# Kernel tuning notes

Measured on AMD Instinct MI355X. Metric: run time of the kernel, lower is better.

## Reference

```python
import jax, jax.numpy as jnp
import numpy as np

GAMMA = 2          # relu(cos_sim)**gamma, from init gamma=2
EPS = 1e-8         # torch CosineSimilarity eps (norm clamp)
B, C, H, WID = 4, 256, 64, 64


def setup_inputs() -> dict:
    key = jax.random.key(0)
    kx, kw = jax.random.split(key)
    x = jax.random.normal(kx, (B, C, H, WID), dtype=jnp.float32)
    # 1x1 conv (nlayers=1): weight [C_out, C_in], bias [C_out]
    W = jax.random.normal(kw, (C, C), dtype=jnp.float32) * 0.02
    b = jnp.zeros((C,), dtype=jnp.float32)
    return {"x": x, "W": W, "b": b}


def reference(x, W, b):
    # x: [B,C,H,W]. Flatten pixels: p/q index (h*W+w).
    Bs, Cs, Hs, Ws = x.shape
    xf = x.reshape(Bs, Cs, Hs * Ws)                      # [B,C,P]
    norm = jnp.sqrt(jnp.sum(xf * xf, axis=1, keepdims=True))
    xn = xf / jnp.maximum(norm, EPS)                     # channel-normalized
    # full pairwise cosine similarity over pixels, relu, power gamma
    s = jax.nn.relu(jnp.einsum('bcp,bcq->bpq', xn, xn)) ** GAMMA  # [B,P,Q]
    # transform: 1x1 conv = per-pixel linear map over channels
    gx = jnp.einsum('oc,bcp->bop', W, xf) + b[None, :, None]      # [B,C,P]
    # y[b,c,p] = sum_q s[b,p,q] * gx[b,c,q]  (== 'bijhw,bchw->bcij')
    y = jnp.einsum('bpq,bcq->bcp', s, gx)
    return y.reshape(Bs, Cs, Hs, Ws)
```

## Files before the change

kernel.cpp:

```cpp
#include <hip/hip_runtime.h>
#include <hip/hip_fp16.h>

#define BN 4
#define CN 256
#define PN 4096
#define QT 64
#define TSTR 264

typedef __attribute__((ext_vector_type(8))) short short8;
typedef __attribute__((ext_vector_type(8))) unsigned short ushort8;
typedef __attribute__((ext_vector_type(4))) unsigned short us4;
typedef __attribute__((ext_vector_type(4))) float f32x4;
typedef __attribute__((ext_vector_type(4))) unsigned int u32x4;
typedef unsigned int u32;

__device__ __forceinline__ unsigned short f2bf(float f) {
  u32 u = __builtin_bit_cast(u32, f);
  return (unsigned short)((u + 0x7fffu + ((u >> 16) & 1u)) >> 16);
}

__device__ __forceinline__ void async_copy16(const void* g, void* l) {
  __builtin_amdgcn_global_load_lds((const __attribute__((address_space(1))) u32*)g,
                                   (__attribute__((address_space(3))) u32*)l, 16, 0, 0);
}


__global__ __launch_bounds__(256) void k_nxgx(const float* __restrict__ x,
                                              const float* __restrict__ Wm,
                                              const float* __restrict__ bias,
                                              unsigned short* __restrict__ xnK,
                                              unsigned short* __restrict__ gxF) {
  __shared__ unsigned short tl[64 * TSTR];
  __shared__ float red[4][64];
  __shared__ float mnl[64];
  const int b = blockIdx.y, qb = blockIdx.x, p0 = qb * 64;
  const int tid = threadIdx.x;
  const int tp = tid & 63, cg = tid >> 6;

  {
    const float* xp = x + ((size_t)b * CN + cg * 64) * PN + p0 + tp;
    float v[64];
    float ss = 0.f;
#pragma unroll
    for (int i = 0; i < 64; ++i) {
      v[i] = xp[(size_t)i * PN];
      ss += v[i] * v[i];
    }
    red[cg][tp] = ss;
    __syncthreads();
    float nrm = sqrtf(red[0][tp] + red[1][tp] + red[2][tp] + red[3][tp]);
    float mn = fmaxf(nrm, 1e-8f);
    float rn = 1.f / mn;
    if (cg == 0) mnl[tp] = mn;
    unsigned int* tl32 = (unsigned int*)tl;
#pragma unroll
    for (int j = 0; j < 32; ++j) {
      unsigned int w = (unsigned int)f2bf(v[2 * j] * rn) |
                       ((unsigned int)f2bf(v[2 * j + 1] * rn) << 16);
      tl32[tp * (TSTR / 2) + cg * 32 + j] = w;
    }
    __syncthreads();
    char* dstb = (char*)xnK + (size_t)b * (PN * CN * 2) + (size_t)qb * 32768;
#pragma unroll
    for (int m = 0; m < 8; ++m) {
      int idx = m * 256 + tid;
      int F = idx >> 6, ln = idx & 63;
      int pl = (F >> 3) * 16 + (ln & 15);
      int ch = (F & 7) * 32 + (ln >> 4) * 8;
      ushort8 o = *(const ushort8*)(tl + pl * TSTR + ch);
      *(ushort8*)(dstb + (size_t)idx * 16) = o;
    }
  }

  const int wave = tid >> 6, lane = tid & 63;
  const int lr = lane & 15, g = lane >> 4;
  char* vbb = (char*)gxF + (size_t)b * (PN * CN * 2) + (size_t)qb * 32768;
#pragma unroll
  for (int mp = 0; mp < 2; ++mp) {
    short8 af[2][8];
#pragma unroll
    for (int mt = 0; mt < 2; ++mt) {
      const float* wr = Wm + (size_t)(wave * 64 + mp * 32 + mt * 16 + lr) * CN;
#pragma unroll
      for (int k = 0; k < 8; ++k) {
        const float* ap = wr + k * 32 + g * 8;
        short8 a;
#pragma unroll
        for (int j = 0; j < 8; ++j) a[j] = (short)f2bf(ap[j]);
        af[mt][k] = a;
      }
    }
    f32x4 acc[2][4];
#pragma unroll
    for (int mt = 0; mt < 2; ++mt)
#pragma unroll
      for (int n = 0; n < 4; ++n) acc[mt][n] = (f32x4){0.f, 0.f, 0.f, 0.f};
#pragma unroll
    for (int n = 0; n < 4; ++n)
#pragma unroll
      for (int k = 0; k < 8; ++k) {
        short8 bf = *(const short8*)((const char*)tl + (n * 16 + lr) * (TSTR * 2) + k * 64 + g * 16);
        acc[0][n] = __builtin_amdgcn_mfma_f32_16x16x32_bf16(af[0][k], bf, acc[0][n], 0, 0, 0);
        acc[1][n] = __builtin_amdgcn_mfma_f32_16x16x32_bf16(af[1][k], bf, acc[1][n], 0, 0, 0);
      }
#pragma unroll
    for (int n = 0; n < 4; ++n) {
      float mn = mnl[n * 16 + lr];
      int kk = n >> 1;
      int q32 = (n & 1) * 16 + lr;
      int gp = (q32 >> 2) & 3;
      int j = ((q32 >> 4) & 1) * 4 + (q32 & 3);
#pragma unroll
      for (int mt = 0; mt < 2; ++mt)
#pragma unroll
        for (int i = 0; i < 4; ++i) {
          int c = wave * 64 + mp * 32 + mt * 16 + g * 4 + i;
          float v = acc[mt][n][i] * mn + bias[c];
          *(unsigned short*)(vbb + ((kk * 16 + (c >> 4)) << 10) + (gp << 8) + ((c & 15) << 4) + (j << 1)) = f2bf(v);
        }
    }
  }
}

extern __shared__ char smem[];

__global__ __launch_bounds__(512, 2) void k_attn(const unsigned short* __restrict__ xnK,
                                                 const unsigned short* __restrict__ gxF,
                                                 __half* __restrict__ p0h, __half* __restrict__ p1h,
                                                 __half* __restrict__ p2h, __half* __restrict__ p3h,
                                                 int lq, int ntiles) {
  const int fid = blockIdx.x;
  const int b = fid & 3;
  const int qs = (fid >> 2) & ((1 << lq) - 1);
  const int pblk = fid >> (2 + lq);
  const int tid = threadIdx.x;
  const int wave = tid >> 6, lane = tid & 63, lr = lane & 15, g = lane >> 4;
  const int qb0 = (qs * (PN >> lq)) >> 6;
  const int p0 = pblk * 256 + wave * 32;
  __half* dsth = (qs == 0) ? p0h : (qs == 1) ? p1h : (qs == 2) ? p2h : p3h;

  const char* xb = (const char*)xnK + (size_t)b * (PN * CN * 2);
  const char* vg = (const char*)gxF + (size_t)b * (PN * CN * 2);
  const char* kq = xb + (size_t)qb0 * 32768;
  const char* vq = vg + (size_t)qb0 * 32768;
  const int ldst = tid * 16;
  const int lane16 = lane * 16;

  auto issue_K = [&](int t) {
    char* kb = smem + (t & 1) * 65536;
    const char* s = kq + (size_t)t * 32768 + ldst;
#pragma unroll
    for (int j = 0; j < 4; ++j) async_copy16(s + j * 8192, kb + ldst + j * 8192);
  };
  auto issue_V = [&](int t) {
    char* vb = smem + (t & 1) * 65536 + 32768;
    const char* s = vq + (size_t)t * 32768 + ldst;
#pragma unroll
    for (int j = 0; j < 4; ++j) async_copy16(s + j * 8192, vb + ldst + j * 8192);
  };

  issue_K(0);
  issue_V(0);

  short8 qf[2][8];
  {
    const char* qpb = xb + (size_t)(pblk * 4 + (wave >> 1)) * 32768;
#pragma unroll
    for (int mt = 0; mt < 2; ++mt) {
      int ntp = (wave & 1) * 2 + mt;
#pragma unroll
      for (int k = 0; k < 8; ++k)
        qf[mt][k] = *(const short8*)(qpb + ((ntp * 8 + k) << 10) + ((g * 16 + lr) << 4));
    }
  }

  f32x4 yacc[2][16];
#pragma unroll
  for (int mt = 0; mt < 2; ++mt)
#pragma unroll
    for (int n = 0; n < 16; ++n) yacc[mt][n] = (f32x4){0.f, 0.f, 0.f, 0.f};

  for (int t = 0; t < ntiles; ++t) {
    const char* kb = smem + (t & 1) * 65536;
    const char* vb = kb + 32768;

    asm volatile("s_waitcnt vmcnt(4)" ::: "memory");
    __builtin_amdgcn_s_barrier();
    if (t + 1 < ntiles) { issue_K(t + 1); issue_V(t + 1); }

    u32 pa[2][2][4];
#pragma unroll
    for (int nh = 0; nh < 2; ++nh) {
      f32x4 sacc[2][2];
#pragma unroll
      for (int n0 = 0; n0 < 2; ++n0)
#pragma unroll
        for (int mt = 0; mt < 2; ++mt) sacc[n0][mt] = (f32x4){0.f, 0.f, 0.f, 0.f};
      __builtin_amdgcn_s_setprio(1);
#pragma unroll
      for (int k = 0; k < 8; ++k) {
        short8 kf0 = *(const short8*)(kb + ((2 * nh) * 8 + k) * 1024 + lane16);
        short8 kf1 = *(const short8*)(kb + ((2 * nh + 1) * 8 + k) * 1024 + lane16);
        sacc[0][0] = __builtin_amdgcn_mfma_f32_16x16x32_bf16(kf0, qf[0][k], sacc[0][0], 0, 0, 0);
        sacc[0][1] = __builtin_amdgcn_mfma_f32_16x16x32_bf16(kf0, qf[1][k], sacc[0][1], 0, 0, 0);
        sacc[1][0] = __builtin_amdgcn_mfma_f32_16x16x32_bf16(kf1, qf[0][k], sacc[1][0], 0, 0, 0);
        sacc[1][1] = __builtin_amdgcn_mfma_f32_16x16x32_bf16(kf1, qf[1][k], sacc[1][1], 0, 0, 0);
      }
      __builtin_amdgcn_s_setprio(0);
#pragma unroll
      for (int mt = 0; mt < 2; ++mt)
#pragma unroll
        for (int n0 = 0; n0 < 2; ++n0)
#pragma unroll
          for (int h = 0; h < 2; ++h) {
            float a0 = fmaxf(sacc[n0][mt][2 * h], 0.f); a0 *= a0;
            float a1 = fmaxf(sacc[n0][mt][2 * h + 1], 0.f); a1 *= a1;
            u32 w;
            asm("v_cvt_pk_bf16_f32 %0, %1, %2" : "=v"(w) : "v"(a0), "v"(a1));
            pa[mt][nh][n0 * 2 + h] = w;
          }
    }

    if (t + 1 < ntiles) {
      asm volatile("s_waitcnt vmcnt(8)" ::: "memory");
    } else {
      asm volatile("s_waitcnt vmcnt(0)" ::: "memory");
    }
    __builtin_amdgcn_s_barrier();

#pragma unroll
    for (int kk = 0; kk < 2; ++kk) {
      u32x4 w0 = {pa[0][kk][0], pa[0][kk][1], pa[0][kk][2], pa[0][kk][3]};
      u32x4 w1 = {pa[1][kk][0], pa[1][kk][1], pa[1][kk][2], pa[1][kk][3]};
      short8 a0 = __builtin_bit_cast(short8, w0);
      short8 a1 = __builtin_bit_cast(short8, w1);
      __builtin_amdgcn_s_setprio(1);
#pragma unroll
      for (int n2 = 0; n2 < 16; ++n2) {
        short8 vf = *(const short8*)(vb + (kk * 16 + n2) * 1024 + lane16);
        yacc[0][n2] = __builtin_amdgcn_mfma_f32_16x16x32_bf16(a0, vf, yacc[0][n2], 0, 0, 0);
        yacc[1][n2] = __builtin_amdgcn_mfma_f32_16x16x32_bf16(a1, vf, yacc[1][n2], 0, 0, 0);
      }
      __builtin_amdgcn_s_setprio(0);
    }
  }
  __builtin_amdgcn_s_barrier();

  float* yl = (float*)(smem + wave * 16384);
  const int row8 = lane >> 3, p4 = (lane & 7) << 2;
#pragma unroll
  for (int cc = 0; cc < 4; ++cc) {
#pragma unroll
    for (int nn = 0; nn < 4; ++nn)
#pragma unroll
      for (int mt = 0; mt < 2; ++mt)
#pragma unroll
        for (int i = 0; i < 4; ++i)
          yl[(nn * 16 + lr) * 33 + mt * 16 + g * 4 + i] = yacc[mt][cc * 4 + nn][i];
#pragma unroll
    for (int r2 = 0; r2 < 8; ++r2) {
      int c = r2 * 8 + row8;
      float4 v = *(const float4*)(yl + c * 33 + p4);
      size_t off = ((size_t)b * CN + cc * 64 + c) * PN + p0 + p4;
      us4 h;
      h[0] = __builtin_bit_cast(unsigned short, __float2half(v.x));
      h[1] = __builtin_bit_cast(unsigned short, __float2half(v.y));
      h[2] = __builtin_bit_cast(unsigned short, __float2half(v.z));
      h[3] = __builtin_bit_cast(unsigned short, __float2half(v.w));
      *(us4*)(dsth + off) = h;
    }
  }
}

__global__ void k_add(float* __restrict__ o, const uint2* __restrict__ a,
                      const uint2* __restrict__ bb, const uint2* __restrict__ c,
                      const uint2* __restrict__ d, int np, int n4) {
  int i = blockIdx.x * blockDim.x + threadIdx.x;
  int stride = gridDim.x * blockDim.x;
  float4* o4 = (float4*)o;
  for (; i < n4; i += stride) {
    uint2 ua = a[i];
    float2 f0 = __half22float2(__builtin_bit_cast(__half2, ua.x));
    float2 f1 = __half22float2(__builtin_bit_cast(__half2, ua.y));
    float4 r = {f0.x, f0.y, f1.x, f1.y};
    uint2 ub = bb[i];
    f0 = __half22float2(__builtin_bit_cast(__half2, ub.x));
    f1 = __half22float2(__builtin_bit_cast(__half2, ub.y));
    r.x += f0.x; r.y += f0.y; r.z += f1.x; r.w += f1.y;
    if (np > 2) {
      uint2 uc = c[i];
      f0 = __half22float2(__builtin_bit_cast(__half2, uc.x));
      f1 = __half22float2(__builtin_bit_cast(__half2, uc.y));
      r.x += f0.x; r.y += f0.y; r.z += f1.x; r.w += f1.y;
      uint2 ud = d[i];
      f0 = __half22float2(__builtin_bit_cast(__half2, ud.x));
      f1 = __half22float2(__builtin_bit_cast(__half2, ud.y));
      r.x += f0.x; r.y += f0.y; r.z += f1.x; r.w += f1.y;
    }
    o4[i] = r;
  }
}

extern "C" void kernel_launch(void* const* d_in, const int* in_sizes, int n_in,
                              void* d_out, int out_size, void* d_ws, size_t ws_size,
                              hipStream_t stream) {
  const float* x = (const float*)d_in[0];
  const float* Wm = (const float*)d_in[1];
  const float* bias = (const float*)d_in[2];
  float* out = (float*)d_out;

  char* ws = (char*)d_ws;
  unsigned short* xnK = (unsigned short*)ws;
  unsigned short* gxF = (unsigned short*)(ws + (size_t)8388608);
  __half* p0 = (__half*)(ws + (size_t)16777216);
  __half* p1 = p0 + 4194304;
  __half* p2 = p1 + 4194304;
  __half* p3 = p2 + 4194304;
  const size_t need4 = 16777216ULL + 4ULL * 8388608ULL;

  hipFuncSetAttribute(reinterpret_cast<const void*>(k_attn),
                      hipFuncAttributeMaxDynamicSharedMemorySize, 131072);

  k_nxgx<<<dim3(PN / 64, BN), 256, 0, stream>>>(x, Wm, bias, xnK, gxF);
  if (ws_size >= need4) {
    k_attn<<<dim3(256), 512, 131072, stream>>>(xnK, gxF, p0, p1, p2, p3, 2, (PN / 4) / QT);
    k_add<<<dim3(1024), 256, 0, stream>>>(out, (const uint2*)p0, (const uint2*)p1,
                                          (const uint2*)p2, (const uint2*)p3, 4, BN * CN * PN / 4);
  } else {
    k_attn<<<dim3(128), 512, 131072, stream>>>(xnK, gxF, p0, p1, p0, p1, 1, (PN / 2) / QT);
    k_add<<<dim3(1024), 256, 0, stream>>>(out, (const uint2*)p0, (const uint2*)p1,
                                          (const uint2*)p0, (const uint2*)p1, 2, BN * CN * PN / 4);
  }
}
```

Measured before the change: 94.67 us.

## Shrink attention tiles to 16 pixels per wave and 32-key tiles for occupancy

Each wave now owns 16 query pixels instead of 32, and key/value tiles are 32 pixels instead of 64. Shared memory per block halves to 64KB, the grid doubles, and launch bounds request 4 blocks per CU. The goal is to fit more waves per CU and spread work over more blocks. In exchange, each K/V fragment loaded from LDS is reused by half as many MFMAs, the loop runs more iterations with more barriers, and the pipeline now waits with vmcnt(0) at every tile, so the loads for the next tile get less overlap.

After: 100.3 us. 5.9% more time.

```diff
diff --git a/kernel.cpp b/kernel.cpp
--- a/kernel.cpp
+++ b/kernel.cpp
@@ -4,7 +4,7 @@
 #define BN 4
 #define CN 256
 #define PN 4096
-#define QT 64
+#define QT 32
 #define TSTR 264
 
 typedef __attribute__((ext_vector_type(8))) short short8;
@@ -33,12 +33,12 @@
   __shared__ unsigned short tl[64 * TSTR];
   __shared__ float red[4][64];
   __shared__ float mnl[64];
-  const int b = blockIdx.y, qb = blockIdx.x, p0 = qb * 64;
+  const int b = blockIdx.y, qb = blockIdx.x;
   const int tid = threadIdx.x;
   const int tp = tid & 63, cg = tid >> 6;
 
   {
-    const float* xp = x + ((size_t)b * CN + cg * 64) * PN + p0 + tp;
+    const float* xp = x + ((size_t)b * CN + cg * 64) * PN + qb * 64 + tp;
     float v[64];
     float ss = 0.f;
 #pragma unroll
@@ -124,7 +124,7 @@
 
 extern __shared__ char smem[];
 
-__global__ __launch_bounds__(512, 2) void k_attn(const unsigned short* __restrict__ xnK,
+__global__ __launch_bounds__(512, 4) void k_attn(const unsigned short* __restrict__ xnK,
                                                  const unsigned short* __restrict__ gxF,
                                                  __half* __restrict__ p0h, __half* __restrict__ p1h,
                                                  __half* __restrict__ p2h, __half* __restrict__ p3h,
@@ -135,133 +135,100 @@
   const int pblk = fid >> (2 + lq);
   const int tid = threadIdx.x;
   const int wave = tid >> 6, lane = tid & 63, lr = lane & 15, g = lane >> 4;
-  const int qb0 = (qs * (PN >> lq)) >> 6;
-  const int p0 = pblk * 256 + wave * 32;
+  const int qt0 = (qs * (PN >> lq)) >> 5;
+  const int p0 = pblk * 128 + wave * 16;
   __half* dsth = (qs == 0) ? p0h : (qs == 1) ? p1h : (qs == 2) ? p2h : p3h;
 
   const char* xb = (const char*)xnK + (size_t)b * (PN * CN * 2);
   const char* vg = (const char*)gxF + (size_t)b * (PN * CN * 2);
-  const char* kq = xb + (size_t)qb0 * 32768;
-  const char* vq = vg + (size_t)qb0 * 32768;
+  const char* kq = xb + (size_t)qt0 * 16384;
+  const char* vq = vg + (size_t)qt0 * 16384;
   const int ldst = tid * 16;
   const int lane16 = lane * 16;
 
-  auto issue_K = [&](int t) {
-    char* kb = smem + (t & 1) * 65536;
-    const char* s = kq + (size_t)t * 32768 + ldst;
-#pragma unroll
-    for (int j = 0; j < 4; ++j) async_copy16(s + j * 8192, kb + ldst + j * 8192);
+  auto issue = [&](int t) {
+    char* kb = smem + (t & 1) * 32768;
+    const char* ks = kq + (size_t)t * 16384 + ldst;
+    const char* vs = vq + (size_t)t * 16384 + ldst;
+    async_copy16(ks, kb + ldst);
+    async_copy16(ks + 8192, kb + ldst + 8192);
+    async_copy16(vs, kb + 16384 + ldst);
+    async_copy16(vs + 8192, kb + 16384 + ldst + 8192);
   };
-  auto issue_V = [&](int t) {
-    char* vb = smem + (t & 1) * 65536 + 32768;
-    const char* s = vq + (size_t)t * 32768 + ldst;
-#pragma unroll
-    for (int j = 0; j < 4; ++j) async_copy16(s + j * 8192, vb + ldst + j * 8192);
-  };
-
-  issue_K(0);
-  issue_V(0);
-
-  short8 qf[2][8];
+
+  issue(0);
+
+  short8 qf[8];
   {
-    const char* qpb = xb + (size_t)(pblk * 4 + (wave >> 1)) * 32768;
-#pragma unroll
-    for (int mt = 0; mt < 2; ++mt) {
-      int ntp = (wave & 1) * 2 + mt;
-#pragma unroll
-      for (int k = 0; k < 8; ++k)
-        qf[mt][k] = *(const short8*)(qpb + ((ntp * 8 + k) << 10) + ((g * 16 + lr) << 4));
-    }
-  }
-
-  f32x4 yacc[2][16];
-#pragma unroll
-  for (int mt = 0; mt < 2; ++mt)
-#pragma unroll
-    for (int n = 0; n < 16; ++n) yacc[mt][n] = (f32x4){0.f, 0.f, 0.f, 0.f};
+    const char* qpb = xb + (size_t)(pblk * 2 + (wave >> 2)) * 32768;
+    const int ntp = wave & 3;
+#pragma unroll
+    for (int k = 0; k < 8; ++k)
+      qf[k] = *(const short8*)(qpb + ((ntp * 8 + k) << 10) + ((g * 16 + lr) << 4));
+  }
+
+  f32x4 yacc[16];
+#pragma unroll
+  for (int n = 0; n < 16; ++n) yacc[n] = (f32x4){0.f, 0.f, 0.f, 0.f};
 
   for (int t = 0; t < ntiles; ++t) {
-    const char* kb = smem + (t & 1) * 65536;
-    const char* vb = kb + 32768;
-
-    asm volatile("s_waitcnt vmcnt(4)" ::: "memory");
+    const char* kb = smem + (t & 1) * 32768;
+    const char* vb = kb + 16384;
+
+    asm volatile("s_waitcnt vmcnt(0)" ::: "memory");
     __builtin_amdgcn_s_barrier();
-    if (t + 1 < ntiles) { issue_K(t + 1); issue_V(t + 1); }
-
-    u32 pa[2][2][4];
-#pragma unroll
-    for (int nh = 0; nh < 2; ++nh) {
-      f32x4 sacc[2][2];
-#pragma unroll
-      for (int n0 = 0; n0 < 2; ++n0)
-#pragma unroll
-        for (int mt = 0; mt < 2; ++mt) sacc[n0][mt] = (f32x4){0.f, 0.f, 0.f, 0.f};
-      __builtin_amdgcn_s_setprio(1);
-#pragma unroll
-      for (int k = 0; k < 8; ++k) {
-        short8 kf0 = *(const short8*)(kb + ((2 * nh) * 8 + k) * 1024 + lane16);
-        short8 kf1 = *(const short8*)(kb + ((2 * nh + 1) * 8 + k) * 1024 + lane16);
-        sacc[0][0] = __builtin_amdgcn_mfma_f32_16x16x32_bf16(kf0, qf[0][k], sacc[0][0], 0, 0, 0);
-        sacc[0][1] = __builtin_amdgcn_mfma_f32_16x16x32_bf16(kf0, qf[1][k], sacc[0][1], 0, 0, 0);
-        sacc[1][0] = __builtin_amdgcn_mfma_f32_16x16x32_bf16(kf1, qf[0][k], sacc[1][0], 0, 0, 0);
-        sacc[1][1] = __builtin_amdgcn_mfma_f32_16x16x32_bf16(kf1, qf[1][k], sacc[1][1], 0, 0, 0);
-      }
-      __builtin_amdgcn_s_setprio(0);
-#pragma unroll
-      for (int mt = 0; mt < 2; ++mt)
-#pragma unroll
-        for (int n0 = 0; n0 < 2; ++n0)
-#pragma unroll
-          for (int h = 0; h < 2; ++h) {
-            float a0 = fmaxf(sacc[n0][mt][2 * h], 0.f); a0 *= a0;
-            float a1 = fmaxf(sacc[n0][mt][2 * h + 1], 0.f); a1 *= a1;
-            u32 w;
-            asm("v_cvt_pk_bf16_f32 %0, %1, %2" : "=v"(w) : "v"(a0), "v"(a1));
-            pa[mt][nh][n0 * 2 + h] = w;
-          }
-    }
-
-    if (t + 1 < ntiles) {
-      asm volatile("s_waitcnt vmcnt(8)" ::: "memory");
-    } else {
-      asm volatile("s_waitcnt vmcnt(0)" ::: "memory");
-    }
-    __builtin_amdgcn_s_barrier();
-
-#pragma unroll
-    for (int kk = 0; kk < 2; ++kk) {
-      u32x4 w0 = {pa[0][kk][0], pa[0][kk][1], pa[0][kk][2], pa[0][kk][3]};
-      u32x4 w1 = {pa[1][kk][0], pa[1][kk][1], pa[1][kk][2], pa[1][kk][3]};
-      short8 a0 = __builtin_bit_cast(short8, w0);
-      short8 a1 = __builtin_bit_cast(short8, w1);
-      __builtin_amdgcn_s_setprio(1);
-#pragma unroll
-      for (int n2 = 0; n2 < 16; ++n2) {
-        short8 vf = *(const short8*)(vb + (kk * 16 + n2) * 1024 + lane16);
-        yacc[0][n2] = __builtin_amdgcn_mfma_f32_16x16x32_bf16(a0, vf, yacc[0][n2], 0, 0, 0);
-        yacc[1][n2] = __builtin_amdgcn_mfma_f32_16x16x32_bf16(a1, vf, yacc[1][n2], 0, 0, 0);
-      }
-      __builtin_amdgcn_s_setprio(0);
-    }
-  }
+    if (t + 1 < ntiles) issue(t + 1);
+
+    f32x4 sacc0 = (f32x4){0.f, 0.f, 0.f, 0.f};
+    f32x4 sacc1 = (f32x4){0.f, 0.f, 0.f, 0.f};
+    __builtin_amdgcn_s_setprio(1);
+#pragma unroll
+    for (int k = 0; k < 8; ++k) {
+      short8 kf0 = *(const short8*)(kb + k * 1024 + lane16);
+      short8 kf1 = *(const short8*)(kb + (8 + k) * 1024 + lane16);
+      sacc0 = __builtin_amdgcn_mfma_f32_16x16x32_bf16(kf0, qf[k], sacc0, 0, 0, 0);
+      sacc1 = __builtin_amdgcn_mfma_f32_16x16x32_bf16(kf1, qf[k], sacc1, 0, 0, 0);
+    }
+    __builtin_amdgcn_s_setprio(0);
+
+    u32 pa[4];
+#pragma unroll
+    for (int h = 0; h < 2; ++h) {
+      float a0 = fmaxf(sacc0[2 * h], 0.f); a0 *= a0;
+      float a1 = fmaxf(sacc0[2 * h + 1], 0.f); a1 *= a1;
+      asm("v_cvt_pk_bf16_f32 %0, %1, %2" : "=v"(pa[h]) : "v"(a0), "v"(a1));
+      float b0 = fmaxf(sacc1[2 * h], 0.f); b0 *= b0;
+      float b1 = fmaxf(sacc1[2 * h + 1], 0.f); b1 *= b1;
+      asm("v_cvt_pk_bf16_f32 %0, %1, %2" : "=v"(pa[2 + h]) : "v"(b0), "v"(b1));
+    }
+    u32x4 w0 = {pa[0], pa[1], pa[2], pa[3]};
+    short8 a0 = __builtin_bit_cast(short8, w0);
+
+    __builtin_amdgcn_s_setprio(1);
+#pragma unroll
+    for (int n2 = 0; n2 < 16; ++n2) {
+      short8 vf = *(const short8*)(vb + n2 * 1024 + lane16);
+      yacc[n2] = __builtin_amdgcn_mfma_f32_16x16x32_bf16(a0, vf, yacc[n2], 0, 0, 0);
+    }
+    __builtin_amdgcn_s_setprio(0);
+  }
+  asm volatile("s_waitcnt vmcnt(0)" ::: "memory");
   __builtin_amdgcn_s_barrier();
 
-  float* yl = (float*)(smem + wave * 16384);
-  const int row8 = lane >> 3, p4 = (lane & 7) << 2;
+  float* yl = (float*)(smem + wave * 8192);
+  const int cq = lane >> 2, pq = (lane & 3) << 2;
 #pragma unroll
   for (int cc = 0; cc < 4; ++cc) {
 #pragma unroll
     for (int nn = 0; nn < 4; ++nn)
 #pragma unroll
-      for (int mt = 0; mt < 2; ++mt)
-#pragma unroll
-        for (int i = 0; i < 4; ++i)
-          yl[(nn * 16 + lr) * 33 + mt * 16 + g * 4 + i] = yacc[mt][cc * 4 + nn][i];
-#pragma unroll
-    for (int r2 = 0; r2 < 8; ++r2) {
-      int c = r2 * 8 + row8;
-      float4 v = *(const float4*)(yl + c * 33 + p4);
-      size_t off = ((size_t)b * CN + cc * 64 + c) * PN + p0 + p4;
+      for (int i = 0; i < 4; ++i)
+        yl[(nn * 16 + lr) * 17 + g * 4 + i] = yacc[cc * 4 + nn][i];
+#pragma unroll
+    for (int i2 = 0; i2 < 4; ++i2) {
+      int c = i2 * 16 + cq;
+      float4 v = *(const float4*)(yl + c * 17 + pq);
+      size_t off = ((size_t)b * CN + cc * 64 + c) * PN + p0 + pq;
       us4 h;
       h[0] = __builtin_bit_cast(unsigned short, __float2half(v.x));
       h[1] = __builtin_bit_cast(unsigned short, __float2half(v.y));
@@ -319,15 +286,15 @@
   const size_t need4 = 16777216ULL + 4ULL * 8388608ULL;
 
   hipFuncSetAttribute(reinterpret_cast<const void*>(k_attn),
-                      hipFuncAttributeMaxDynamicSharedMemorySize, 131072);
+                      hipFuncAttributeMaxDynamicSharedMemorySize, 65536);
 
   k_nxgx<<<dim3(PN / 64, BN), 256, 0, stream>>>(x, Wm, bias, xnK, gxF);
   if (ws_size >= need4) {
-    k_attn<<<dim3(256), 512, 131072, stream>>>(xnK, gxF, p0, p1, p2, p3, 2, (PN / 4) / QT);
+    k_attn<<<dim3(512), 512, 65536, stream>>>(xnK, gxF, p0, p1, p2, p3, 2, (PN / 4) / QT);
     k_add<<<dim3(1024), 256, 0, stream>>>(out, (const uint2*)p0, (const uint2*)p1,
                                           (const uint2*)p2, (const uint2*)p3, 4, BN * CN * PN / 4);
   } else {
-    k_attn<<<dim3(128), 512, 131072, stream>>>(xnK, gxF, p0, p1, p0, p1, 1, (PN / 2) / QT);
+    k_attn<<<dim3(256), 512, 65536, stream>>>(xnK, gxF, p0, p1, p0, p1, 1, (PN / 2) / QT);
     k_add<<<dim3(1024), 256, 0, stream>>>(out, (const uint2*)p0, (const uint2*)p1,
                                           (const uint2*)p0, (const uint2*)p1, 2, BN * CN * PN / 4);
   }
```
